# Kernel tuning notes

Measured on AMD Instinct MI355X. Metric: run time of the kernel, lower is better.

Reference implementation:

```python
import jax, jax.numpy as jnp
import numpy as np

HIDDEN = 1024
FEAT = 64
BATCH = 512
SEQ = 64
EPS = 1e-5


def _gru_layer(x_seq, Wih, Whh, bih, bhh):
    # x_seq: [B,T,Din]; Wih: [3H,Din]; Whh: [3H,H]; gate order r,z,n (PyTorch)
    B = x_seq.shape[0]
    H = Whh.shape[1]
    gates_x = jnp.einsum('btd,gd->btg', x_seq, Wih) + bih  # [B,T,3H]
    h0 = jnp.zeros((B, H), x_seq.dtype)

    def step(h, gx):
        gh = h @ Whh.T + bhh                       # [B,3H]
        xr, xz, xn = jnp.split(gx, 3, axis=-1)
        hr, hz, hn = jnp.split(gh, 3, axis=-1)
        r = jax.nn.sigmoid(xr + hr)
        z = jax.nn.sigmoid(xz + hz)
        n = jnp.tanh(xn + r * hn)
        h_new = (1.0 - z) * n + z * h
        return h_new, h_new

    _, ys = jax.lax.scan(step, h0, jnp.swapaxes(gates_x, 0, 1))  # [T,B,H]
    return jnp.swapaxes(ys, 0, 1)                                # [B,T,H]


def setup_inputs() -> dict:
    key = jax.random.key(0)
    ks = jax.random.split(key, 20)
    s = 1.0 / np.sqrt(HIDDEN)
    u = lambda k, shape: jax.random.uniform(k, shape, jnp.float32, -s, s)
    inp = {
        'x': jax.random.normal(ks[0], (BATCH, SEQ, FEAT), jnp.float32),
        'Wih0': u(ks[1], (3 * HIDDEN, FEAT)),
        'Whh0': u(ks[2], (3 * HIDDEN, HIDDEN)),
        'bih0': u(ks[3], (3 * HIDDEN,)),
        'bhh0': u(ks[4], (3 * HIDDEN,)),
        'Wih1': u(ks[5], (3 * HIDDEN, HIDDEN)),
        'Whh1': u(ks[6], (3 * HIDDEN, HIDDEN)),
        'bih1': u(ks[7], (3 * HIDDEN,)),
        'bhh1': u(ks[8], (3 * HIDDEN,)),
        'Wih2': u(ks[9], (3 * HIDDEN, HIDDEN)),
        'Whh2': u(ks[10], (3 * HIDDEN, HIDDEN)),
        'bih2': u(ks[11], (3 * HIDDEN,)),
        'bhh2': u(ks[12], (3 * HIDDEN,)),
        'gamma': jnp.ones((HIDDEN,), jnp.float32),
        'beta': jnp.zeros((HIDDEN,), jnp.float32),
        'fcW': u(ks[13], (1, HIDDEN)),
        'fcb': u(ks[14], (1,)),
    }
    return inp


def reference(x, Wih0, Whh0, bih0, bhh0, Wih1, Whh1, bih1, bhh1,
              Wih2, Whh2, bih2, bhh2, gamma, beta, fcW, fcb):
    h = _gru_layer(x, Wih0, Whh0, bih0, bhh0)
    h = _gru_layer(h, Wih1, Whh1, bih1, bhh1)
    h = _gru_layer(h, Wih2, Whh2, bih2, bhh2)
    out = h[:, -1, :]                               # [B,H] last timestep
    # BatchNorm1d in training mode: biased batch stats (B != 1 branch)
    mu = jnp.mean(out, axis=0)
    var = jnp.mean((out - mu) ** 2, axis=0)
    out = (out - mu) * jax.lax.rsqrt(var + EPS) * gamma + beta
    out = out @ fcW.T + fcb                         # [B,1]
    return jax.nn.sigmoid(out)[:, 0]                # [B]
```

## Files before the change

### kernel.cpp

```cpp
#include <hip/hip_runtime.h>
#include <hip/hip_bf16.h>
#include <stdint.h>

#define HIDDEN 1024
#define FEAT   64
#define BATCH  512
#define SEQ    64
#define GATES  3072

typedef __attribute__((ext_vector_type(4))) float f32x4;
typedef __attribute__((ext_vector_type(8))) short s16x8;

#define MFMA16(a, b, c) __builtin_amdgcn_mfma_f32_16x16x32_bf16(a, b, c, 0, 0, 0)

__device__ inline unsigned short f2bf(float f) {
    unsigned u = __builtin_bit_cast(unsigned, f);
    u += 0x7fff + ((u >> 16) & 1);
    return (unsigned short)(u >> 16);
}
__device__ inline float bf2f(unsigned short s) {
    unsigned u = ((unsigned)s) << 16;
    return __builtin_bit_cast(float, u);
}

#define GLOAD_LDS16(g, l) __builtin_amdgcn_global_load_lds( \
    (const __attribute__((address_space(1))) unsigned int*)(g), \
    (__attribute__((address_space(3))) unsigned int*)(l), 16, 0, 0)

__global__ void k_conv_whh(const float* __restrict__ src, unsigned short* __restrict__ dst) {
    int i = blockIdx.x * 256 + threadIdx.x;
    int d = i >> 10, k = i & 1023;
    int ub = d / 48, rem = d - ub * 48;
    int g = rem >> 4, jj = rem & 15;
    int srow = g * 1024 + ub * 16 + jj;
    dst[i] = f2bf(src[(size_t)srow * 1024 + k]);
}

__global__ void k_conv_wih0(const float* __restrict__ src, unsigned short* __restrict__ dst) {
    int i = blockIdx.x * 256 + threadIdx.x;
    int d = i >> 6, k = i & 63;
    int ub = d / 48, rem = d - ub * 48;
    int g = rem >> 4, jj = rem & 15;
    int srow = g * 1024 + ub * 16 + jj;
    dst[i] = f2bf(src[(size_t)srow * 64 + k]);
}

__global__ void k_xpose(const float* __restrict__ x, unsigned short* __restrict__ xbf) {
    int i = blockIdx.x * blockDim.x + threadIdx.x;
    if (i >= BATCH * SEQ * FEAT) return;
    int f = i & 63, t = (i >> 6) & 63, b = i >> 12;
    xbf[((size_t)t * BATCH + b) * FEAT + f] = f2bf(x[i]);
}

__device__ __forceinline__ void stage_chunk(const char* src, int rowStride,
                                            unsigned short* dstL, int nKB, int wid, int lane)
{
    const int lrow = lane >> 3;
    const int lcol = lane & 7;
    for (int g = wid; g < nKB; g += 4) {
        int row = g * 8 + lrow;
        int col16 = lcol ^ (row & 7);
        GLOAD_LDS16(src + (size_t)row * rowStride + col16 * 16, (char*)dstL + (g << 10));
    }
}

template<int NSLOT>
__device__ __forceinline__ void compute_chunk(const unsigned short* aL, const unsigned short* wL,
                                              int wid, int lane, f32x4 (&acc)[2][4])
{
    const int l15 = lane & 15, hi = lane >> 4;
    const int swz = (l15 & 7) << 4;
    const char* ap = (const char*)aL;
    const char* wp = (const char*)wL;
#pragma unroll
    for (int ks = 0; ks < 2; ++ks) {
        const int kb = ks * 64 + (hi << 4);
        s16x8 a0 = *(const s16x8*)(ap + ((((wid * 32 + l15) * 128) + kb) ^ swz));
        s16x8 a1 = *(const s16x8*)(ap + ((((wid * 32 + 16 + l15) * 128) + kb) ^ swz));
        s16x8 b0 = *(const s16x8*)(wp + (((l15 * 128) + kb) ^ swz));
        s16x8 b1 = *(const s16x8*)(wp + ((((16 + l15) * 128) + kb) ^ swz));
        s16x8 b2 = *(const s16x8*)(wp + ((((32 + l15) * 128) + kb) ^ swz));
        acc[0][0]     = MFMA16(a0, b0, acc[0][0]);
        acc[0][1]     = MFMA16(a0, b1, acc[0][1]);
        acc[0][NSLOT] = MFMA16(a0, b2, acc[0][NSLOT]);
        acc[1][0]     = MFMA16(a1, b0, acc[1][0]);
        acc[1][1]     = MFMA16(a1, b1, acc[1][1]);
        acc[1][NSLOT] = MFMA16(a1, b2, acc[1][NSLOT]);
    }
}

__global__ __launch_bounds__(256, 3) void k_stage(
    int d,
    const unsigned short* __restrict__ xbf,
    unsigned short* __restrict__ h0,
    unsigned short* __restrict__ h1,
    unsigned short* __restrict__ h2,
    const unsigned short* __restrict__ wih0R,
    const unsigned short* __restrict__ whh0R,
    const unsigned short* __restrict__ wih1R,
    const unsigned short* __restrict__ whh1R,
    const unsigned short* __restrict__ wih2R,
    const unsigned short* __restrict__ whh2R,
    const float* __restrict__ bih0, const float* __restrict__ bhh0,
    const float* __restrict__ bih1, const float* __restrict__ bhh1,
    const float* __restrict__ bih2, const float* __restrict__ bhh2)
{
    __shared__ unsigned short Wb[2][48 * 64];
    __shared__ unsigned short Ab[2][128 * 64];
    const int bid = blockIdx.x;
    const int slot = bid & 7;
    const int p = (bid >> 3) % 24;
    const int bg = bid / 192;
    const int pair = slot + 8 * p;
    const int layer = pair >> 6;
    const int ub = pair & 63;
    const int t = d - layer;
    if (t < 0 || t >= SEQ) return;

    const int tid = threadIdx.x;
    const int wid = tid >> 6, lane = tid & 63;
    const int l15 = lane & 15, hi = lane >> 4;
    const int brow0 = bg * 128;

    const unsigned short* inseq = (layer == 0) ? xbf : ((layer == 1) ? h0 : h1);
    unsigned short* outseq = (layer == 0) ? h0 : ((layer == 1) ? h1 : h2);
    const unsigned short* wihR = (layer == 0) ? wih0R : ((layer == 1) ? wih1R : wih2R);
    const unsigned short* whhR = (layer == 0) ? whh0R : ((layer == 1) ? whh1R : whh2R);

    const int aStride1 = (layer == 0) ? 128 : 2048;
    const char* a1base = (layer == 0)
        ? (const char*)xbf + (size_t)t * BATCH * FEAT * 2 + (size_t)brow0 * 128
        : (const char*)inseq + (size_t)t * BATCH * HIDDEN * 2 + (size_t)brow0 * 2048;
    const char* w1base = (layer == 0)
        ? (const char*)wihR + (size_t)ub * 48 * 64 * 2
        : (const char*)wihR + (size_t)ub * 48 * 1024 * 2;
    const int wStride1 = (layer == 0) ? 128 : 2048;
    const char* a2base = (const char*)outseq + (size_t)(t - 1) * BATCH * HIDDEN * 2 + (size_t)brow0 * 2048;
    const char* w2base = (const char*)whhR + (size_t)ub * 48 * 1024 * 2;

    const int NCH1 = (layer == 0) ? 1 : 16;
    const int NCH2 = (t > 0) ? 16 : 0;

    f32x4 acc[2][4];
    const f32x4 zero = {0.f, 0.f, 0.f, 0.f};
#pragma unroll
    for (int i = 0; i < 2; ++i)
#pragma unroll
        for (int s = 0; s < 4; ++s) acc[i][s] = zero;

    int cur = 0;
    stage_chunk(w1base, wStride1, Wb[0], 6, wid, lane);
    stage_chunk(a1base, aStride1, Ab[0], 16, wid, lane);
    __syncthreads();

    for (int c = 0; c < NCH1; ++c) {
        int nxt = cur ^ 1;
        if (c + 1 < NCH1) {
            stage_chunk(w1base + (c + 1) * 128, wStride1, Wb[nxt], 6, wid, lane);
            stage_chunk(a1base + (c + 1) * 128, aStride1, Ab[nxt], 16, wid, lane);
        } else if (NCH2 > 0) {
            stage_chunk(w2base, 2048, Wb[nxt], 6, wid, lane);
            stage_chunk(a2base, 2048, Ab[nxt], 16, wid, lane);
        }
        compute_chunk<2>(Ab[cur], Wb[cur], wid, lane, acc);
        __syncthreads();
        cur = nxt;
    }
    for (int c = 0; c < NCH2; ++c) {
        int nxt = cur ^ 1;
        if (c + 1 < NCH2) {
            stage_chunk(w2base + (c + 1) * 128, 2048, Wb[nxt], 6, wid, lane);
            stage_chunk(a2base + (c + 1) * 128, 2048, Ab[nxt], 16, wid, lane);
        }
        compute_chunk<3>(Ab[cur], Wb[cur], wid, lane, acc);
        __syncthreads();
        cur = nxt;
    }

    const float* bih = (layer == 0) ? bih0 : ((layer == 1) ? bih1 : bih2);
    const float* bhh = (layer == 0) ? bhh0 : ((layer == 1) ? bhh1 : bhh2);
    const int j = ub * 16 + l15;
    const float br  = bih[j] + bhh[j];
    const float bz  = bih[HIDDEN + j] + bhh[HIDDEN + j];
    const float bxn = bih[2 * HIDDEN + j];
    const float bhn = bhh[2 * HIDDEN + j];
    const unsigned short* hprev = outseq + (size_t)((t > 0) ? (t - 1) : 0) * (BATCH * HIDDEN);
    unsigned short* hout = outseq + (size_t)t * (BATCH * HIDDEN);
#pragma unroll
    for (int i = 0; i < 2; ++i)
#pragma unroll
        for (int r = 0; r < 4; ++r) {
            int brow = brow0 + wid * 32 + i * 16 + hi * 4 + r;
            size_t hidx = (size_t)brow * HIDDEN + j;
            float rg = 1.f / (1.f + __expf(-(acc[i][0][r] + br)));
            float zg = 1.f / (1.f + __expf(-(acc[i][1][r] + bz)));
            float ng = tanhf(acc[i][2][r] + bxn + rg * (acc[i][3][r] + bhn));
            float hv = (t > 0) ? bf2f(hprev[hidx]) : 0.f;
            float hnew = (1.f - zg) * ng + zg * hv;
            hout[hidx] = f2bf(hnew);
        }
}

__global__ void k_bn_part(const unsigned short* __restrict__ h, float* __restrict__ part) {
    int j = threadIdx.x;
    int blk = blockIdx.x;
    float s = 0.f, q = 0.f;
    for (int b = blk * 32; b < blk * 32 + 32; ++b) {
        float v = bf2f(h[(size_t)b * HIDDEN + j]);
        s += v; q += v * v;
    }
    part[blk * 2048 + j] = s;
    part[blk * 2048 + 1024 + j] = q;
}

__global__ void k_bn_fold(const float* __restrict__ part, const float* __restrict__ gamma,
                          const float* __restrict__ beta, float* __restrict__ a, float* __restrict__ bb)
{
    int j = blockIdx.x * 256 + threadIdx.x;
    float s = 0.f, q = 0.f;
    for (int p = 0; p < 16; ++p) {
        s += part[p * 2048 + j];
        q += part[p * 2048 + 1024 + j];
    }
    float mu = s * (1.f / BATCH);
    float var = q * (1.f / BATCH) - mu * mu;
    float rs = rsqrtf(var + 1e-5f);
    float aj = gamma[j] * rs;
    a[j] = aj;
    bb[j] = beta[j] - mu * aj;
}

__global__ void k_fc(const unsigned short* __restrict__ h, const float* __restrict__ a, const float* __restrict__ bb,
                     const float* __restrict__ fcW, const float* __restrict__ fcb, float* __restrict__ out)
{
    int b = blockIdx.x;
    int lane = threadIdx.x;
    float s = 0.f;
    for (int j = lane; j < HIDDEN; j += 64)
        s += (bf2f(h[(size_t)b * HIDDEN + j]) * a[j] + bb[j]) * fcW[j];
#pragma unroll
    for (int m = 32; m; m >>= 1) s += __shfl_xor(s, m, 64);
    if (lane == 0) out[b] = 1.f / (1.f + __expf(-(s + fcb[0])));
}

extern "C" void kernel_launch(void* const* d_in, const int* in_sizes, int n_in,
                              void* d_out, int out_size, void* d_ws, size_t ws_size,
                              hipStream_t stream)
{
    const float* x = (const float*)d_in[0];
    const float* W_ih[3] = {(const float*)d_in[1], (const float*)d_in[5], (const float*)d_in[9]};
    const float* W_hh[3] = {(const float*)d_in[2], (const float*)d_in[6], (const float*)d_in[10]};
    const float* b_ih[3] = {(const float*)d_in[3], (const float*)d_in[7], (const float*)d_in[11]};
    const float* b_hh[3] = {(const float*)d_in[4], (const float*)d_in[8], (const float*)d_in[12]};
    const float* gamma = (const float*)d_in[13];
    const float* beta  = (const float*)d_in[14];
    const float* fcW   = (const float*)d_in[15];
    const float* fcb   = (const float*)d_in[16];

    char* ws = (char*)d_ws;
    size_t off = 0;
    auto alloc = [&](size_t bytes) -> void* {
        void* p = ws + off;
        off = (off + bytes + 255) & ~(size_t)255;
        return p;
    };
    unsigned short* wih0R = (unsigned short*)alloc((size_t)GATES * FEAT * 2);
    unsigned short* whh0R = (unsigned short*)alloc((size_t)GATES * HIDDEN * 2);
    unsigned short* wih1R = (unsigned short*)alloc((size_t)GATES * HIDDEN * 2);
    unsigned short* whh1R = (unsigned short*)alloc((size_t)GATES * HIDDEN * 2);
    unsigned short* wih2R = (unsigned short*)alloc((size_t)GATES * HIDDEN * 2);
    unsigned short* whh2R = (unsigned short*)alloc((size_t)GATES * HIDDEN * 2);
    unsigned short* xbf = (unsigned short*)alloc((size_t)SEQ * BATCH * FEAT * 2);
    unsigned short* h0  = (unsigned short*)alloc((size_t)SEQ * BATCH * HIDDEN * 2);
    unsigned short* h1  = (unsigned short*)alloc((size_t)SEQ * BATCH * HIDDEN * 2);
    unsigned short* h2  = (unsigned short*)alloc((size_t)SEQ * BATCH * HIDDEN * 2);
    float* part = (float*)alloc(16 * 2048 * 4);
    float* abuf = (float*)alloc(HIDDEN * 4);
    float* bbuf = (float*)alloc(HIDDEN * 4);

    k_conv_wih0<<<(GATES * FEAT) / 256, 256, 0, stream>>>(W_ih[0], wih0R);
    k_conv_whh<<<(GATES * HIDDEN) / 256, 256, 0, stream>>>(W_hh[0], whh0R);
    k_conv_whh<<<(GATES * HIDDEN) / 256, 256, 0, stream>>>(W_ih[1], wih1R);
    k_conv_whh<<<(GATES * HIDDEN) / 256, 256, 0, stream>>>(W_hh[1], whh1R);
    k_conv_whh<<<(GATES * HIDDEN) / 256, 256, 0, stream>>>(W_ih[2], wih2R);
    k_conv_whh<<<(GATES * HIDDEN) / 256, 256, 0, stream>>>(W_hh[2], whh2R);
    k_xpose<<<(BATCH * SEQ * FEAT + 255) / 256, 256, 0, stream>>>(x, xbf);

    for (int d = 0; d < SEQ + 2; ++d)
        k_stage<<<768, 256, 0, stream>>>(d, xbf, h0, h1, h2,
                                         wih0R, whh0R, wih1R, whh1R, wih2R, whh2R,
                                         b_ih[0], b_hh[0], b_ih[1], b_hh[1], b_ih[2], b_hh[2]);

    const unsigned short* hlast = h2 + (size_t)(SEQ - 1) * (BATCH * HIDDEN);
    k_bn_part<<<16, 1024, 0, stream>>>(hlast, part);
    k_bn_fold<<<HIDDEN / 256, 256, 0, stream>>>(part, gamma, beta, abuf, bbuf);
    k_fc<<<BATCH, 64, 0, stream>>>(hlast, abuf, bbuf, fcW, fcb, (float*)d_out);
}
```

Baseline: 2.287 ms.

## Load activations directly to registers, widen K chunks, use 8 waves per block

The GRU step kernel no longer stages the activation tile through LDS. Each wave loads its 16 batch rows straight into registers, while only the weight tile is staged in LDS, now in 256-wide K chunks (4 chunks instead of 16). Blocks grow from 4 to 8 waves, each computing 16 rows instead of 32. This cuts LDS traffic, the number of barriers and the LDS footprint, at the cost of more register pressure from holding A fragments and uncoalesced per-lane global loads.

Result: slower. 4.554 ms (+99.1%).

```diff
diff --git a/kernel.cpp b/kernel.cpp
--- a/kernel.cpp
+++ b/kernel.cpp
@@ -52,44 +52,69 @@
     xbf[((size_t)t * BATCH + b) * FEAT + f] = f2bf(x[i]);
 }
 
-__device__ __forceinline__ void stage_chunk(const char* src, int rowStride,
-                                            unsigned short* dstL, int nKB, int wid, int lane)
-{
-    const int lrow = lane >> 3;
-    const int lcol = lane & 7;
-    for (int g = wid; g < nKB; g += 4) {
-        int row = g * 8 + lrow;
-        int col16 = lcol ^ (row & 7);
-        GLOAD_LDS16(src + (size_t)row * rowStride + col16 * 16, (char*)dstL + (g << 10));
-    }
+__device__ __forceinline__ void stage_w24(const char* src, unsigned short* dstL, int wid, int lane)
+{
+#pragma unroll
+    for (int r = 0; r < 3; ++r) {
+        int g = wid * 3 + r;
+        int row = g * 2 + (lane >> 5);
+        int col16 = (lane & 31) ^ (row & 7);
+        GLOAD_LDS16(src + (size_t)row * 2048 + col16 * 16, (char*)dstL + (g << 10));
+    }
+}
+
+__device__ __forceinline__ void stage_x6(const char* src, unsigned short* dstL, int wid, int lane)
+{
+    if (wid < 6) {
+        int row = wid * 8 + (lane >> 3);
+        int col16 = (lane & 7) ^ (row & 7);
+        GLOAD_LDS16(src + (size_t)row * 128 + col16 * 16, (char*)dstL + (wid << 10));
+    }
+}
+
+__device__ __forceinline__ void loadA8(const char* pa, s16x8 (&v)[8]) {
+#pragma unroll
+    for (int ks = 0; ks < 8; ++ks) v[ks] = *(const s16x8*)(pa + ks * 64);
 }
 
 template<int NSLOT>
-__device__ __forceinline__ void compute_chunk(const unsigned short* aL, const unsigned short* wL,
-                                              int wid, int lane, f32x4 (&acc)[2][4])
+__device__ __forceinline__ void compute24(const s16x8 (&a)[8], const unsigned short* wL,
+                                          int lane, f32x4 (&acc)[4])
 {
     const int l15 = lane & 15, hi = lane >> 4;
     const int swz = (l15 & 7) << 4;
-    const char* ap = (const char*)aL;
     const char* wp = (const char*)wL;
 #pragma unroll
+    for (int ks = 0; ks < 8; ++ks) {
+        int kb = ks * 64 + (hi << 4);
+        s16x8 b0 = *(const s16x8*)(wp + (((l15)      * 512 + kb) ^ swz));
+        s16x8 b1 = *(const s16x8*)(wp + (((16 + l15) * 512 + kb) ^ swz));
+        s16x8 b2 = *(const s16x8*)(wp + (((32 + l15) * 512 + kb) ^ swz));
+        acc[0]     = MFMA16(a[ks], b0, acc[0]);
+        acc[1]     = MFMA16(a[ks], b1, acc[1]);
+        acc[NSLOT] = MFMA16(a[ks], b2, acc[NSLOT]);
+    }
+}
+
+__device__ __forceinline__ void compute_x(const s16x8 (&a)[2], const unsigned short* wL,
+                                          int lane, f32x4 (&acc)[4])
+{
+    const int l15 = lane & 15, hi = lane >> 4;
+    const int swz = (l15 & 7) << 4;
+    const char* wp = (const char*)wL;
+#pragma unroll
     for (int ks = 0; ks < 2; ++ks) {
-        const int kb = ks * 64 + (hi << 4);
-        s16x8 a0 = *(const s16x8*)(ap + ((((wid * 32 + l15) * 128) + kb) ^ swz));
-        s16x8 a1 = *(const s16x8*)(ap + ((((wid * 32 + 16 + l15) * 128) + kb) ^ swz));
-        s16x8 b0 = *(const s16x8*)(wp + (((l15 * 128) + kb) ^ swz));
-        s16x8 b1 = *(const s16x8*)(wp + ((((16 + l15) * 128) + kb) ^ swz));
-        s16x8 b2 = *(const s16x8*)(wp + ((((32 + l15) * 128) + kb) ^ swz));
-        acc[0][0]     = MFMA16(a0, b0, acc[0][0]);
-        acc[0][1]     = MFMA16(a0, b1, acc[0][1]);
-        acc[0][NSLOT] = MFMA16(a0, b2, acc[0][NSLOT]);
-        acc[1][0]     = MFMA16(a1, b0, acc[1][0]);
-        acc[1][1]     = MFMA16(a1, b1, acc[1][1]);
-        acc[1][NSLOT] = MFMA16(a1, b2, acc[1][NSLOT]);
-    }
-}
-
-__global__ __launch_bounds__(256, 3) void k_stage(
+        int kb = ks * 64 + (hi << 4);
+        s16x8 b0 = *(const s16x8*)(wp + (((l15)      * 128 + kb) ^ swz));
+        s16x8 b1 = *(const s16x8*)(wp + (((16 + l15) * 128 + kb) ^ swz));
+        s16x8 b2 = *(const s16x8*)(wp + (((32 + l15) * 128 + kb) ^ swz));
+        acc[0] = MFMA16(a[ks], b0, acc[0]);
+        acc[1] = MFMA16(a[ks], b1, acc[1]);
+        acc[2] = MFMA16(a[ks], b2, acc[2]);
+    }
+}
+
+__global__ __launch_bounds__(512, 6) void k_stage(
     int d,
     const unsigned short* __restrict__ xbf,
     unsigned short* __restrict__ h0,
@@ -105,8 +130,7 @@
     const float* __restrict__ bih1, const float* __restrict__ bhh1,
     const float* __restrict__ bih2, const float* __restrict__ bhh2)
 {
-    __shared__ unsigned short Wb[2][48 * 64];
-    __shared__ unsigned short Ab[2][128 * 64];
+    __shared__ unsigned short Wb[2][48 * 256];
     const int bid = blockIdx.x;
     const int slot = bid & 7;
     const int p = (bid >> 3) % 24;
@@ -121,60 +145,73 @@
     const int wid = tid >> 6, lane = tid & 63;
     const int l15 = lane & 15, hi = lane >> 4;
     const int brow0 = bg * 128;
+    const int arow = brow0 + wid * 16 + l15;
 
     const unsigned short* inseq = (layer == 0) ? xbf : ((layer == 1) ? h0 : h1);
     unsigned short* outseq = (layer == 0) ? h0 : ((layer == 1) ? h1 : h2);
     const unsigned short* wihR = (layer == 0) ? wih0R : ((layer == 1) ? wih1R : wih2R);
     const unsigned short* whhR = (layer == 0) ? whh0R : ((layer == 1) ? whh1R : whh2R);
 
-    const int aStride1 = (layer == 0) ? 128 : 2048;
-    const char* a1base = (layer == 0)
-        ? (const char*)xbf + (size_t)t * BATCH * FEAT * 2 + (size_t)brow0 * 128
-        : (const char*)inseq + (size_t)t * BATCH * HIDDEN * 2 + (size_t)brow0 * 2048;
-    const char* w1base = (layer == 0)
-        ? (const char*)wihR + (size_t)ub * 48 * 64 * 2
-        : (const char*)wihR + (size_t)ub * 48 * 1024 * 2;
-    const int wStride1 = (layer == 0) ? 128 : 2048;
-    const char* a2base = (const char*)outseq + (size_t)(t - 1) * BATCH * HIDDEN * 2 + (size_t)brow0 * 2048;
-    const char* w2base = (const char*)whhR + (size_t)ub * 48 * 1024 * 2;
-
-    const int NCH1 = (layer == 0) ? 1 : 16;
-    const int NCH2 = (t > 0) ? 16 : 0;
-
-    f32x4 acc[2][4];
+    const char* w2 = (const char*)whhR + (size_t)ub * 48 * 1024 * 2;
+    const char* a2 = (const char*)outseq + ((size_t)(t - 1) * BATCH * HIDDEN + (size_t)arow * HIDDEN) * 2 + (hi << 4);
+
+    f32x4 acc[4];
     const f32x4 zero = {0.f, 0.f, 0.f, 0.f};
 #pragma unroll
-    for (int i = 0; i < 2; ++i)
-#pragma unroll
-        for (int s = 0; s < 4; ++s) acc[i][s] = zero;
-
-    int cur = 0;
-    stage_chunk(w1base, wStride1, Wb[0], 6, wid, lane);
-    stage_chunk(a1base, aStride1, Ab[0], 16, wid, lane);
-    __syncthreads();
-
-    for (int c = 0; c < NCH1; ++c) {
-        int nxt = cur ^ 1;
-        if (c + 1 < NCH1) {
-            stage_chunk(w1base + (c + 1) * 128, wStride1, Wb[nxt], 6, wid, lane);
-            stage_chunk(a1base + (c + 1) * 128, aStride1, Ab[nxt], 16, wid, lane);
-        } else if (NCH2 > 0) {
-            stage_chunk(w2base, 2048, Wb[nxt], 6, wid, lane);
-            stage_chunk(a2base, 2048, Ab[nxt], 16, wid, lane);
+    for (int s = 0; s < 4; ++s) acc[s] = zero;
+
+    s16x8 rA[2][8];
+
+    if (layer == 0) {
+        const char* xrow = (const char*)xbf + ((size_t)t * BATCH * FEAT + (size_t)arow * FEAT) * 2 + (hi << 4);
+        s16x8 ax[2];
+        ax[0] = *(const s16x8*)(xrow);
+        ax[1] = *(const s16x8*)(xrow + 64);
+        stage_x6((const char*)wih0R + (size_t)ub * 48 * 64 * 2, Wb[0], wid, lane);
+        if (t > 0) { stage_w24(w2, Wb[1], wid, lane); loadA8(a2, rA[1]); }
+        __syncthreads();
+        compute_x(ax, Wb[0], lane, acc);
+        if (t > 0) {
+            __syncthreads();
+#pragma unroll
+            for (int c = 0; c < 4; ++c) {
+                if (c < 3) {
+                    stage_w24(w2 + (c + 1) * 512, Wb[c & 1], wid, lane);
+                    loadA8(a2 + (c + 1) * 512, rA[c & 1]);
+                }
+                compute24<3>(rA[(c + 1) & 1], Wb[(c + 1) & 1], lane, acc);
+                if (c < 3) __syncthreads();
+            }
         }
-        compute_chunk<2>(Ab[cur], Wb[cur], wid, lane, acc);
+    } else {
+        const char* w1 = (const char*)wihR + (size_t)ub * 48 * 1024 * 2;
+        const char* a1 = (const char*)inseq + ((size_t)t * BATCH * HIDDEN + (size_t)arow * HIDDEN) * 2 + (hi << 4);
+        stage_w24(w1, Wb[0], wid, lane);
+        loadA8(a1, rA[0]);
         __syncthreads();
-        cur = nxt;
-    }
-    for (int c = 0; c < NCH2; ++c) {
-        int nxt = cur ^ 1;
-        if (c + 1 < NCH2) {
-            stage_chunk(w2base + (c + 1) * 128, 2048, Wb[nxt], 6, wid, lane);
-            stage_chunk(a2base + (c + 1) * 128, 2048, Ab[nxt], 16, wid, lane);
+#pragma unroll
+        for (int c = 0; c < 4; ++c) {
+            if (c < 3) {
+                stage_w24(w1 + (c + 1) * 512, Wb[(c + 1) & 1], wid, lane);
+                loadA8(a1 + (c + 1) * 512, rA[(c + 1) & 1]);
+            } else if (t > 0) {
+                stage_w24(w2, Wb[0], wid, lane);
+                loadA8(a2, rA[0]);
+            }
+            compute24<2>(rA[c & 1], Wb[c & 1], lane, acc);
+            if (c < 3 || t > 0) __syncthreads();
         }
-        compute_chunk<3>(Ab[cur], Wb[cur], wid, lane, acc);
-        __syncthreads();
-        cur = nxt;
+        if (t > 0) {
+#pragma unroll
+            for (int c = 0; c < 4; ++c) {
+                if (c < 3) {
+                    stage_w24(w2 + (c + 1) * 512, Wb[(c + 1) & 1], wid, lane);
+                    loadA8(a2 + (c + 1) * 512, rA[(c + 1) & 1]);
+                }
+                compute24<3>(rA[c & 1], Wb[c & 1], lane, acc);
+                if (c < 3) __syncthreads();
+            }
+        }
     }
 
     const float* bih = (layer == 0) ? bih0 : ((layer == 1) ? bih1 : bih2);
@@ -187,18 +224,16 @@
     const unsigned short* hprev = outseq + (size_t)((t > 0) ? (t - 1) : 0) * (BATCH * HIDDEN);
     unsigned short* hout = outseq + (size_t)t * (BATCH * HIDDEN);
 #pragma unroll
-    for (int i = 0; i < 2; ++i)
-#pragma unroll
-        for (int r = 0; r < 4; ++r) {
-            int brow = brow0 + wid * 32 + i * 16 + hi * 4 + r;
-            size_t hidx = (size_t)brow * HIDDEN + j;
-            float rg = 1.f / (1.f + __expf(-(acc[i][0][r] + br)));
-            float zg = 1.f / (1.f + __expf(-(acc[i][1][r] + bz)));
-            float ng = tanhf(acc[i][2][r] + bxn + rg * (acc[i][3][r] + bhn));
-            float hv = (t > 0) ? bf2f(hprev[hidx]) : 0.f;
-            float hnew = (1.f - zg) * ng + zg * hv;
-            hout[hidx] = f2bf(hnew);
-        }
+    for (int rr = 0; rr < 4; ++rr) {
+        int brow = brow0 + wid * 16 + hi * 4 + rr;
+        size_t hidx = (size_t)brow * HIDDEN + j;
+        float rg = 1.f / (1.f + __expf(-(acc[0][rr] + br)));
+        float zg = 1.f / (1.f + __expf(-(acc[1][rr] + bz)));
+        float ng = tanhf(acc[2][rr] + bxn + rg * (acc[3][rr] + bhn));
+        float hv = (t > 0) ? bf2f(hprev[hidx]) : 0.f;
+        float hnew = (1.f - zg) * ng + zg * hv;
+        hout[hidx] = f2bf(hnew);
+    }
 }
 
 __global__ void k_bn_part(const unsigned short* __restrict__ h, float* __restrict__ part) {
@@ -287,7 +322,7 @@
     k_xpose<<<(BATCH * SEQ * FEAT + 255) / 256, 256, 0, stream>>>(x, xbf);
 
     for (int d = 0; d < SEQ + 2; ++d)
-        k_stage<<<768, 256, 0, stream>>>(d, xbf, h0, h1, h2,
+        k_stage<<<768, 512, 0, stream>>>(d, xbf, h0, h1, h2,
                                          wih0R, whh0R, wih1R, whh1R, wih2R, whh2R,
                                          b_ih[0], b_hh[0], b_ih[1], b_hh[1], b_ih[2], b_hh[2]);
 
```
